# Kernel optimization log

Hardware: AMD Instinct MI355X
Metric: run time of the kernel (lower is better)

## Reference

```python
import jax, jax.numpy as jnp
import numpy as np

EPS = 1e-12  # torch F.normalize eps

def _l2norm(t):
    # normalize over last axis (tokens N), matching F.normalize(dim=-1)
    n = jnp.sqrt(jnp.sum(t * t, axis=-1, keepdims=True))
    return t / jnp.maximum(n, EPS)

def setup_inputs() -> dict:
    key = jax.random.key(0)
    ks = jax.random.split(key, 4)
    B, N, C, H = 16, 3136, 768, 16
    x = jax.random.normal(ks[0], (B, N, C), dtype=jnp.float32)
    w_qkv = jax.random.normal(ks[1], (3 * C, C), dtype=jnp.float32) * (C ** -0.5)
    temperature = jnp.ones((H, 1, 1), dtype=jnp.float32)
    w_proj = jax.random.normal(ks[2], (C, C), dtype=jnp.float32) * (C ** -0.5)
    b_proj = jnp.zeros((C,), dtype=jnp.float32)
    return {"x": x, "w_qkv": w_qkv, "temperature": temperature,
            "w_proj": w_proj, "b_proj": b_proj}

def reference(x, w_qkv, temperature, w_proj, b_proj):
    B, N, C = x.shape
    H = temperature.shape[0]
    dh = C // H
    # qkv: [B,N,3C] -> [B,N,3,H,dh] -> [3,B,H,dh,N]
    qkv = (x @ w_qkv.T).reshape(B, N, 3, H, dh)
    qkv = jnp.transpose(qkv, (2, 0, 3, 4, 1))
    q, k, v = qkv[0], qkv[1], qkv[2]          # each [B,H,dh,N]
    q = _l2norm(q)
    k = _l2norm(k)
    # cross-covariance attention over channel axis: [B,H,dh,dh]
    attn = jnp.einsum('bhdn,bhen->bhde', q, k) * temperature
    attn = jax.nn.softmax(attn, axis=-1)
    out = jnp.einsum('bhde,bhen->bhdn', attn, v)  # [B,H,dh,N]
    out = jnp.transpose(out, (0, 3, 1, 2)).reshape(B, N, C)
    return out @ w_proj.T + b_proj
```

## Files before the change

### kernel.cpp

```cpp
#include <hip/hip_runtime.h>
#include <hip/hip_bf16.h>
#include <stdint.h>

using f32x4   = __attribute__((ext_vector_type(4))) float;
using half8   = __attribute__((ext_vector_type(8))) _Float16;
using float4v = __attribute__((ext_vector_type(4))) float;

typedef const __attribute__((address_space(1))) void gas_void;
typedef __attribute__((address_space(3))) void las_void;

__device__ __forceinline__ void gload_lds16(const void* gptr, void* lptr) {
  __builtin_amdgcn_global_load_lds((gas_void*)(uintptr_t)gptr,
                                   (las_void*)(uintptr_t)lptr, 16, 0, 0);
}

#define MFMA_F16(a, b, c) __builtin_amdgcn_mfma_f32_16x16x32_f16((a), (b), (c), 0, 0, 0)

__global__ void k_cvt4(const float* __restrict__ x, const float* __restrict__ wqkv,
                       const float* __restrict__ wproj,
                       _Float16* __restrict__ x16, _Float16* __restrict__ w16,
                       _Float16* __restrict__ wp16, _Float16* __restrict__ wvT) {
  const long N0 = 4816896L, N1 = 221184L, N2 = 73728L, N3 = 98304L;
  const long total = N0 + N1 + N2 + N3;
  for (long i = (long)blockIdx.x * blockDim.x + threadIdx.x; i < total;
       i += (long)gridDim.x * blockDim.x) {
    if (i < N0 + N1 + N2) {
      const float* src; _Float16* dst; long off;
      if (i < N0)            { src = x;     dst = x16;  off = i; }
      else if (i < N0 + N1)  { src = wqkv;  dst = w16;  off = i - N0; }
      else                   { src = wproj; dst = wp16; off = i - N0 - N1; }
      const float4v* p = (const float4v*)(src + off * 8);
      float4v a = p[0], b = p[1];
      half8 o;
      o[0] = (_Float16)a[0]; o[1] = (_Float16)a[1]; o[2] = (_Float16)a[2]; o[3] = (_Float16)a[3];
      o[4] = (_Float16)b[0]; o[5] = (_Float16)b[1]; o[6] = (_Float16)b[2]; o[7] = (_Float16)b[3];
      *(half8*)(dst + off * 8) = o;
    } else {
      const long u = i - (N0 + N1 + N2);
      const int h = (int)(u / 6144);
      const int r = (int)(u % 6144);
      const int f = r >> 3, e0 = (r & 7) * 8;
      half8 o;
      if (e0 >= 48) {
#pragma unroll
        for (int j = 0; j < 8; ++j) o[j] = (_Float16)0.f;
      } else {
#pragma unroll
        for (int j = 0; j < 8; ++j)
          o[j] = (_Float16)wqkv[(long)(1536 + h * 48 + e0 + j) * 768 + f];
      }
      *(half8*)(wvT + ((long)(h * 768 + f) * 64 + e0)) = o;
    }
  }
}

template<bool OUT_F32>
__global__ __launch_bounds__(512, 2)
void k_gemm8p(const _Float16* __restrict__ A, const _Float16* __restrict__ B,
              void* __restrict__ Cv, const float* __restrict__ bias,
              int Mt, int Nt, long Areal, long Astr, long Bstr, long Cstr,
              long N, long K)
{
  __shared__ _Float16 lds[65536];
  const int tid  = threadIdx.x;
  const int wv   = tid >> 6, lane = tid & 63;
  const int g    = lane >> 4, cidx = lane & 15;
  const int wr   = wv >> 2, wc = wv & 3;

  const int nwg = (int)gridDim.x;
  const int q = nwg >> 3, r = nwg & 7;
  const int xcd = (int)blockIdx.x & 7, bidx = (int)blockIdx.x >> 3;
  int wg = (xcd < r ? xcd * (q + 1) : r * (q + 1) + (xcd - r) * q) + bidx;

  const int tpb = Mt * Nt;
  const int b   = wg / tpb;
  const int rem = wg - b * tpb;
  const long mt = rem % Mt, nt = rem / Mt;
  const long m0 = mt * 256, n0 = nt * 256;

  const int NT = (int)(K >> 6);
  const int NI = NT >> 1;

  const _Float16* Ab = A + b * Astr + m0 * K;
  const _Float16* Bb = B + b * Bstr + n0 * K;

  const int srow = lane >> 2;
  const int sgr  = (lane & 3) ^ ((lane >> 3) & 3);

  auto stage = [&](int op, int buf, int kh, int t) {
    const _Float16* src = op ? Bb : Ab;
    const long koff = (long)t * 64 + kh * 32 + sgr * 8;
#pragma unroll
    for (int l = 0; l < 2; ++l) {
      const int chunk = l * 8 + wv;
      gload_lds16(src + (long)(chunk * 16 + srow) * K + koff,
                  &lds[buf * 32768 + op * 16384 + kh * 8192 + chunk * 512]);
    }
  };

  const int gr  = (g ^ ((cidx >> 1) & 3)) * 8;
  const int raA = (wr * 128 + cidx) * 32 + gr;
  const int raB = 16384 + (wc * 64 + cidx) * 32 + gr;

  f32x4 acc[8][4] = {};

  stage(0, 0, 0, 0); stage(1, 0, 0, 0);
  stage(0, 0, 1, 0); stage(1, 0, 1, 0);
  stage(0, 1, 0, 1); stage(1, 1, 0, 1);
  asm volatile("s_waitcnt vmcnt(4)" ::: "memory");
  __builtin_amdgcn_sched_barrier(0);
  __builtin_amdgcn_s_barrier();

  half8 afA[4], afB[4], bfA[4], bfB[4];
#pragma unroll
  for (int mm = 0; mm < 4; ++mm) afA[mm] = *(const half8*)&lds[raA + mm * 512];
#pragma unroll
  for (int nn = 0; nn < 4; ++nn) bfA[nn] = *(const half8*)&lds[raB + nn * 512];

#define XPH(CURA, CURB, MLO, NA, NBUF, NKS, NMLO, LOADB, NB, STAGE, BDRY)      \
  {                                                                            \
    STAGE;                                                                     \
    if (BDRY) {                                                                \
      asm volatile("s_waitcnt vmcnt(4)" ::: "memory");                         \
      __builtin_amdgcn_sched_barrier(0);                                       \
    }                                                                          \
    __builtin_amdgcn_s_barrier();                                              \
    _Pragma("unroll")                                                          \
    for (int mm = 0; mm < 4; ++mm)                                             \
      NA[mm] = *(const half8*)&lds[(NBUF)*32768 + (NKS)*8192 + raA + ((NMLO)+mm)*512]; \
    if (LOADB) {                                                               \
      _Pragma("unroll")                                                        \
      for (int nn = 0; nn < 4; ++nn)                                           \
        NB[nn] = *(const half8*)&lds[(NBUF)*32768 + (NKS)*8192 + raB + nn*512]; \
    }                                                                          \
    __builtin_amdgcn_sched_barrier(0);                                         \
    __builtin_amdgcn_s_setprio(1);                                             \
    _Pragma("unroll")                                                          \
    for (int mm = 0; mm < 4; ++mm)                                             \
      _Pragma("unroll")                                                        \
      for (int nn = 0; nn < 4; ++nn)                                           \
        acc[(MLO)+mm][nn] = MFMA_F16(CURA[mm], CURB[nn], acc[(MLO)+mm][nn]);   \
    __builtin_amdgcn_s_setprio(0);                                             \
    __builtin_amdgcn_s_barrier();                                              \
  }

  for (int it = 0; it < NI; ++it) {
    const int t1c = 2 * it + 1;
    int tn2 = 2 * it + 2; if (tn2 >= NT) tn2 -= NT;
    int tn3 = 2 * it + 3; if (tn3 >= NT) tn3 -= NT;
    XPH(afA, bfA, 0, afB, 0, 0, 4, 0, bfB, stage(0, 1, 1, t1c), false)
    XPH(afB, bfA, 4, afA, 0, 1, 0, 1, bfB, stage(1, 1, 1, t1c), false)
    XPH(afA, bfB, 0, afB, 0, 1, 4, 0, bfA, stage(0, 0, 0, tn2), false)
    XPH(afB, bfB, 4, afA, 1, 0, 0, 1, bfA, stage(1, 0, 0, tn2), true )
    XPH(afA, bfA, 0, afB, 1, 0, 4, 0, bfB, stage(0, 0, 1, tn2), false)
    XPH(afB, bfA, 4, afA, 1, 1, 0, 1, bfB, stage(1, 0, 1, tn2), false)
    XPH(afA, bfB, 0, afB, 1, 1, 4, 0, bfA, stage(0, 1, 0, tn3), false)
    XPH(afB, bfB, 4, afA, 0, 0, 0, 1, bfA, stage(1, 1, 0, tn3), true )
  }
#undef XPH

  float bv[4] = {0.f, 0.f, 0.f, 0.f};
  if (bias) {
#pragma unroll
    for (int n = 0; n < 4; ++n) bv[n] = bias[n0 + wc * 64 + n * 16 + cidx];
  }
  if constexpr (OUT_F32) {
    float* C = (float*)Cv + b * Cstr;
#pragma unroll
    for (int m = 0; m < 8; ++m)
#pragma unroll
      for (int rr = 0; rr < 4; ++rr) {
        const long row = m0 + wr * 128 + m * 16 + g * 4 + rr;
        if (row < Areal) {
#pragma unroll
          for (int n = 0; n < 4; ++n)
            C[row * N + (n0 + wc * 64 + n * 16 + cidx)] = acc[m][n][rr] + bv[n];
        }
      }
  } else {
    _Float16* C = (_Float16*)Cv + b * Cstr;
#pragma unroll
    for (int m = 0; m < 8; ++m)
#pragma unroll
      for (int rr = 0; rr < 4; ++rr) {
        const long row = m0 + wr * 128 + m * 16 + g * 4 + rr;
        if (row < Areal) {
#pragma unroll
          for (int n = 0; n < 4; ++n)
            C[row * N + (n0 + wc * 64 + n * 16 + cidx)] = (_Float16)acc[m][n][rr];
        }
      }
  }
}

__global__ __launch_bounds__(256)
void k_wfin(const _Float16* __restrict__ Ag, const _Float16* __restrict__ Bg,
            _Float16* __restrict__ Cg)
{
  __shared__ _Float16 lds[2][2][128 * 32];
  const int tid  = threadIdx.x;
  const int wv   = tid >> 6, lane = tid & 63;
  const int g    = lane >> 4, cidx = lane & 15;
  const int wr   = wv >> 1, wc = wv & 1;

  const int nwg = (int)gridDim.x;
  const int q = nwg >> 3, r = nwg & 7;
  const int xcd = (int)blockIdx.x & 7, bidx = (int)blockIdx.x >> 3;
  const int wg  = (xcd < r ? xcd * (q + 1) : r * (q + 1) + (xcd - r) * q) + bidx;

  const int b = wg / 36, rem = wg % 36;
  const int mt = rem % 6, nt = rem / 6;
  const _Float16* Ab = Ag + (long)mt * 128 * 768;
  const _Float16* Bb = Bg + (long)b * 589824 + (long)nt * 128 * 768;
  _Float16* C = Cg + (long)b * 589824;

  const int srow = lane >> 2;
  const int sgr  = (lane & 3) ^ ((lane >> 3) & 3);

  auto stage = [&](int buf, int kt) {
#pragma unroll
    for (int i = 0; i < 2; ++i) {
      const int chunk = wv * 2 + i;
      const long go = (long)(chunk * 16 + srow) * 768 + (long)kt * 32 + sgr * 8;
      gload_lds16(Ab + go, &lds[buf][0][chunk * 512]);
      gload_lds16(Bb + go, &lds[buf][1][chunk * 512]);
    }
  };

  const int gr = (g ^ ((cidx >> 1) & 3)) * 8;

  f32x4 acc[4][4] = {};
  stage(0, 0);
  __syncthreads();
  for (int kt = 0; kt < 24; ++kt) {
    const int cur = kt & 1;
    if (kt + 1 < 24) stage(cur ^ 1, kt + 1);
    const _Float16* la = &lds[cur][0][0];
    const _Float16* lb = &lds[cur][1][0];
    half8 af[4], bf[4];
#pragma unroll
    for (int m = 0; m < 4; ++m)
      af[m] = *(const half8*)&la[(wr * 64 + m * 16 + cidx) * 32 + gr];
#pragma unroll
    for (int n = 0; n < 4; ++n)
      bf[n] = *(const half8*)&lb[(wc * 64 + n * 16 + cidx) * 32 + gr];
#pragma unroll
    for (int m = 0; m < 4; ++m)
#pragma unroll
      for (int n = 0; n < 4; ++n)
        acc[m][n] = MFMA_F16(af[m], bf[n], acc[m][n]);
    __syncthreads();
  }
#pragma unroll
  for (int m = 0; m < 4; ++m)
#pragma unroll
    for (int rr = 0; rr < 4; ++rr) {
      const long row = mt * 128 + wr * 64 + m * 16 + g * 4 + rr;
#pragma unroll
      for (int n = 0; n < 4; ++n)
        C[row * 768 + (nt * 128 + wc * 64 + n * 16 + cidx)] = (_Float16)acc[m][n][rr];
    }
}

__global__ __launch_bounds__(256)
void k_heads(const _Float16* __restrict__ qk,
             const _Float16* __restrict__ wvT,
             const float* __restrict__ temperature,
             _Float16* __restrict__ weffT)
{
  const int b = blockIdx.x >> 4;
  const int h = blockIdx.x & 15;
  const int tid = threadIdx.x;
  const int w = tid >> 6, lane = tid & 63;
  const int g = lane >> 4, c = lane & 15;
  const long T = 50176;
  const long tb = (long)b * 3136;

  __shared__ float red[4][48 * 48];
  __shared__ float redss[4][2][48];
  __shared__ float inv[2][48];
  __shared__ _Float16 Pb[48 * 64];

  f32x4 sqk[3][3] = {};
  f32x4 sqq[3] = {};
  f32x4 skk[3] = {};

  const _Float16* qbase = qk + (long)(h * 48) * T + tb;
  const _Float16* kbase = qk + (long)(768 + h * 48) * T + tb;

  for (int chunk = w; chunk < 49; chunk += 4) {
    const int t0 = chunk * 64;
    half8 qf[3][2], kf[3][2];
#pragma unroll
    for (int m = 0; m < 3; ++m)
#pragma unroll
      for (int ks = 0; ks < 2; ++ks) {
        const long off = (long)(m * 16 + c) * T + t0 + ks * 32 + g * 8;
        qf[m][ks] = *(const half8*)(qbase + off);
        kf[m][ks] = *(const half8*)(kbase + off);
      }
#pragma unroll
    for (int ks = 0; ks < 2; ++ks)
#pragma unroll
      for (int m = 0; m < 3; ++m) {
        sqq[m] = MFMA_F16(qf[m][ks], qf[m][ks], sqq[m]);
        skk[m] = MFMA_F16(kf[m][ks], kf[m][ks], skk[m]);
#pragma unroll
        for (int n = 0; n < 3; ++n)
          sqk[m][n] = MFMA_F16(qf[m][ks], kf[n][ks], sqk[m][n]);
      }
  }

#pragma unroll
  for (int m = 0; m < 3; ++m) {
#pragma unroll
    for (int n = 0; n < 3; ++n)
#pragma unroll
      for (int r = 0; r < 4; ++r)
        red[w][(m * 16 + g * 4 + r) * 48 + n * 16 + c] = sqk[m][n][r];
#pragma unroll
    for (int r = 0; r < 4; ++r)
      if (c == g * 4 + r) {
        redss[w][0][m * 16 + c] = sqq[m][r];
        redss[w][1][m * 16 + c] = skk[m][r];
      }
  }
  __syncthreads();

  if (tid < 96) {
    const int is_k = tid / 48, d = tid % 48;
    const float s = redss[0][is_k][d] + redss[1][is_k][d] + redss[2][is_k][d] + redss[3][is_k][d];
    inv[is_k][d] = 1.0f / fmaxf(sqrtf(s), 1e-12f);
  }
  __syncthreads();

  if (tid < 48) {
    const int d = tid;
    const float iq = inv[0][d] * temperature[h];
    float rowv[48];
    float mx = -3.0e38f;
#pragma unroll
    for (int e = 0; e < 48; ++e) {
      const int idx = d * 48 + e;
      float t = (red[0][idx] + red[1][idx] + red[2][idx] + red[3][idx]) * iq * inv[1][e];
      rowv[e] = t;
      mx = fmaxf(mx, t);
    }
    float sum = 0.f;
#pragma unroll
    for (int e = 0; e < 48; ++e) {
      const float p = __expf(rowv[e] - mx);
      rowv[e] = p;
      sum += p;
    }
    const float is = 1.0f / sum;
#pragma unroll
    for (int e = 0; e < 48; ++e)
      Pb[d * 64 + e] = (_Float16)(rowv[e] * is);
#pragma unroll
    for (int e = 48; e < 64; ++e)
      Pb[d * 64 + e] = (_Float16)0.f;
  }
  __syncthreads();

  half8 pf[3][2];
#pragma unroll
  for (int nf = 0; nf < 3; ++nf)
#pragma unroll
    for (int ks = 0; ks < 2; ++ks)
      pf[nf][ks] = *(const half8*)&Pb[(nf * 16 + c) * 64 + ks * 32 + g * 8];

  const _Float16* wvh = wvT + (long)h * 768 * 64;
  _Float16* wout = weffT + (long)b * 589824 + h * 48;

  for (int m = 0; m < 12; ++m) {
    const int f0 = w * 192 + m * 16;
    half8 va[2];
#pragma unroll
    for (int ks = 0; ks < 2; ++ks)
      va[ks] = *(const half8*)&wvh[(long)(f0 + c) * 64 + ks * 32 + g * 8];
    f32x4 a3[3] = {};
#pragma unroll
    for (int ks = 0; ks < 2; ++ks)
#pragma unroll
      for (int nf = 0; nf < 3; ++nf)
        a3[nf] = MFMA_F16(va[ks], pf[nf][ks], a3[nf]);
#pragma unroll
    for (int nf = 0; nf < 3; ++nf)
#pragma unroll
      for (int r = 0; r < 4; ++r)
        wout[(long)(f0 + g * 4 + r) * 768 + nf * 16 + c] = (_Float16)a3[nf][r];
  }
}

extern "C" void kernel_launch(void* const* d_in, const int* in_sizes, int n_in,
                              void* d_out, int out_size, void* d_ws, size_t ws_size,
                              hipStream_t stream)
{
  (void)in_sizes; (void)n_in; (void)out_size; (void)ws_size;
  const float* x      = (const float*)d_in[0];
  const float* w_qkv  = (const float*)d_in[1];
  const float* temp   = (const float*)d_in[2];
  const float* w_proj = (const float*)d_in[3];
  const float* b_proj = (const float*)d_in[4];
  float* out = (float*)d_out;

  char* ws = (char*)d_ws;
  _Float16* x16   = (_Float16*)(ws);
  _Float16* qkbuf = (_Float16*)(ws + 77070336L);
  _Float16* weffT = (_Float16*)(ws + 231211008L);
  _Float16* wfin  = (_Float16*)(ws + 250085376L);
  _Float16* w16   = (_Float16*)(ws + 268959744L);
  _Float16* wp16  = (_Float16*)(ws + 272498688L);
  _Float16* wvT   = (_Float16*)(ws + 273678336L);

  k_cvt4<<<2048, 256, 0, stream>>>(x, w_qkv, w_proj, x16, w16, wp16, wvT);
  k_gemm8p<false><<<1176, 512, 0, stream>>>(w16, x16, qkbuf, nullptr,
                                            6, 196, 1536, 0, 0, 0, 50176, 768);
  k_heads<<<256, 256, 0, stream>>>(qkbuf, wvT, temp, weffT);
  k_wfin<<<576, 256, 0, stream>>>(wp16, weffT, wfin);
  k_gemm8p<true><<<624, 512, 0, stream>>>(x16, wfin, out, b_proj,
                                          13, 3, 3136, 3136L * 768, 589824, 3136L * 768,
                                          768, 768);
}
```

Measured before the change: 365.9 us.

## Compute q·k and norms via per-batch Gram matrix of x instead of materializing QK

Replaces the large QK projection GEMM (1536x50176x768) with a per-batch symmetric Gram matrix G = xᵀx (768x768, computed over tokens), then forms Wq·G and Wk·G to get qᵀk and the q/k squared norms algebraically. Adds a transpose-and-convert kernel for x and swaps the 256-tile pipelined GEMM for a simpler 128-tile double-buffered GEMM used for all remaining GEMMs. This cuts the FLOPs and the large qk intermediate traffic, but it loses the hand-tuned pipelined GEMM for the final projection and adds an fp16 Gram accumulation whose precision may be a risk.

```diff
diff --git a/kernel.cpp b/kernel.cpp
--- a/kernel.cpp
+++ b/kernel.cpp
@@ -4,6 +4,7 @@
 
 using f32x4   = __attribute__((ext_vector_type(4))) float;
 using half8   = __attribute__((ext_vector_type(8))) _Float16;
+using half4   = __attribute__((ext_vector_type(4))) _Float16;
 using float4v = __attribute__((ext_vector_type(4))) float;
 
 typedef const __attribute__((address_space(1))) void gas_void;
@@ -16,19 +17,17 @@
 
 #define MFMA_F16(a, b, c) __builtin_amdgcn_mfma_f32_16x16x32_f16((a), (b), (c), 0, 0, 0)
 
-__global__ void k_cvt4(const float* __restrict__ x, const float* __restrict__ wqkv,
-                       const float* __restrict__ wproj,
-                       _Float16* __restrict__ x16, _Float16* __restrict__ w16,
-                       _Float16* __restrict__ wp16, _Float16* __restrict__ wvT) {
-  const long N0 = 4816896L, N1 = 221184L, N2 = 73728L, N3 = 98304L;
-  const long total = N0 + N1 + N2 + N3;
+__global__ void k_cvtw(const float* __restrict__ wqkv, const float* __restrict__ wproj,
+                       _Float16* __restrict__ w16, _Float16* __restrict__ wp16,
+                       _Float16* __restrict__ wvT) {
+  const long N1 = 221184L, N2 = 73728L, N3 = 98304L;
+  const long total = N1 + N2 + N3;
   for (long i = (long)blockIdx.x * blockDim.x + threadIdx.x; i < total;
        i += (long)gridDim.x * blockDim.x) {
-    if (i < N0 + N1 + N2) {
+    if (i < N1 + N2) {
       const float* src; _Float16* dst; long off;
-      if (i < N0)            { src = x;     dst = x16;  off = i; }
-      else if (i < N0 + N1)  { src = wqkv;  dst = w16;  off = i - N0; }
-      else                   { src = wproj; dst = wp16; off = i - N0 - N1; }
+      if (i < N1) { src = wqkv;  dst = w16;  off = i; }
+      else        { src = wproj; dst = wp16; off = i - N1; }
       const float4v* p = (const float4v*)(src + off * 8);
       float4v a = p[0], b = p[1];
       half8 o;
@@ -36,7 +35,7 @@
       o[4] = (_Float16)b[0]; o[5] = (_Float16)b[1]; o[6] = (_Float16)b[2]; o[7] = (_Float16)b[3];
       *(half8*)(dst + off * 8) = o;
     } else {
-      const long u = i - (N0 + N1 + N2);
+      const long u = i - N1 - N2;
       const int h = (int)(u / 6144);
       const int r = (int)(u % 6144);
       const int f = r >> 3, e0 = (r & 7) * 8;
@@ -54,110 +53,182 @@
   }
 }
 
-template<bool OUT_F32>
-__global__ __launch_bounds__(512, 2)
-void k_gemm8p(const _Float16* __restrict__ A, const _Float16* __restrict__ B,
-              void* __restrict__ Cv, const float* __restrict__ bias,
-              int Mt, int Nt, long Areal, long Astr, long Bstr, long Cstr,
-              long N, long K)
-{
-  __shared__ _Float16 lds[65536];
-  const int tid  = threadIdx.x;
-  const int wv   = tid >> 6, lane = tid & 63;
-  const int g    = lane >> 4, cidx = lane & 15;
-  const int wr   = wv >> 2, wc = wv & 3;
+__global__ __launch_bounds__(256)
+void k_cvtx(const float* __restrict__ x, _Float16* __restrict__ x16,
+            _Float16* __restrict__ xT) {
+  __shared__ _Float16 lt[64 * 68];
+  const int bid = blockIdx.x;
+  const int b = bid / 588;
+  const int rem = bid % 588;
+  const int tt = rem / 12, ct = rem % 12;
+  const long t0g = (long)b * 3136 + tt * 64;
+  const int c0 = ct * 64;
+  const int tid = threadIdx.x;
+#pragma unroll
+  for (int ch = 0; ch < 4; ++ch) {
+    const int idx = tid + ch * 256;
+    const int tr = idx >> 4, cg = (idx & 15) * 4;
+    float4v v = *(const float4v*)&x[(t0g + tr) * 768 + c0 + cg];
+    half4 hv;
+    hv[0] = (_Float16)v[0]; hv[1] = (_Float16)v[1];
+    hv[2] = (_Float16)v[2]; hv[3] = (_Float16)v[3];
+    *(half4*)&x16[(t0g + tr) * 768 + c0 + cg] = hv;
+    *(half4*)&lt[tr * 68 + cg] = hv;
+  }
+  __syncthreads();
+  const int c = tid >> 2, tch = tid & 3;
+  half8 o0, o1;
+#pragma unroll
+  for (int j = 0; j < 8; ++j) o0[j] = lt[(tch * 16 + j) * 68 + c];
+#pragma unroll
+  for (int j = 0; j < 8; ++j) o1[j] = lt[(tch * 16 + 8 + j) * 68 + c];
+  _Float16* dst = xT + (long)b * 2408448 + (long)(c0 + c) * 3136 + tt * 64 + tch * 16;
+  *(half8*)dst = o0;
+  *(half8*)(dst + 8) = o1;
+}
+
+__global__ __launch_bounds__(256)
+void k_gram(const _Float16* __restrict__ xT, _Float16* __restrict__ G) {
+  __shared__ _Float16 lds[2][2][128 * 32];
+  const int tid = threadIdx.x;
+  const int wv = tid >> 6, lane = tid & 63;
+  const int g = lane >> 4, cidx = lane & 15;
+  const int wr = wv >> 1, wc = wv & 1;
 
   const int nwg = (int)gridDim.x;
   const int q = nwg >> 3, r = nwg & 7;
   const int xcd = (int)blockIdx.x & 7, bidx = (int)blockIdx.x >> 3;
   int wg = (xcd < r ? xcd * (q + 1) : r * (q + 1) + (xcd - r) * q) + bidx;
-
+  const int b = wg / 21;
+  int p = wg % 21;
+  int mt = 0;
+  while (p >= 6 - mt) { p -= 6 - mt; ++mt; }
+  const int nt = mt + p;
+
+  const _Float16* Ab = xT + (long)b * 2408448 + (long)mt * 128 * 3136;
+  const _Float16* Bb = xT + (long)b * 2408448 + (long)nt * 128 * 3136;
+
+  const int srow = lane >> 2;
+  const int sgr  = (lane & 3) ^ ((lane >> 3) & 3);
+
+  auto stage = [&](int buf, int kt) {
+#pragma unroll
+    for (int l = 0; l < 2; ++l) {
+      const int rbase = wv * 32 + l * 16;
+      const long koff = (long)kt * 32 + sgr * 8;
+      gload_lds16(Ab + (long)(rbase + srow) * 3136 + koff, &lds[buf][0][rbase * 32]);
+      gload_lds16(Bb + (long)(rbase + srow) * 3136 + koff, &lds[buf][1][rbase * 32]);
+    }
+  };
+  const int gr = (g ^ ((cidx >> 1) & 3)) * 8;
+
+  f32x4 acc[4][4] = {};
+  stage(0, 0);
+  __syncthreads();
+  for (int kt = 0; kt < 98; ++kt) {
+    const int cur = kt & 1;
+    if (kt + 1 < 98) stage(cur ^ 1, kt + 1);
+    half8 af[4], bf[4];
+#pragma unroll
+    for (int m = 0; m < 4; ++m)
+      af[m] = *(const half8*)&lds[cur][0][(wr * 64 + m * 16 + cidx) * 32 + gr];
+#pragma unroll
+    for (int n = 0; n < 4; ++n)
+      bf[n] = *(const half8*)&lds[cur][1][(wc * 64 + n * 16 + cidx) * 32 + gr];
+#pragma unroll
+    for (int m = 0; m < 4; ++m)
+#pragma unroll
+      for (int n = 0; n < 4; ++n)
+        acc[m][n] = MFMA_F16(af[m], bf[n], acc[m][n]);
+    __syncthreads();
+  }
+  _Float16* Gb = G + (long)b * 589824;
+  const long m0 = (long)mt * 128, n0 = (long)nt * 128;
+#pragma unroll
+  for (int m = 0; m < 4; ++m)
+#pragma unroll
+    for (int rr = 0; rr < 4; ++rr) {
+      const long row = m0 + wr * 64 + m * 16 + g * 4 + rr;
+#pragma unroll
+      for (int n = 0; n < 4; ++n)
+        Gb[row * 768 + n0 + wc * 64 + n * 16 + cidx] = (_Float16)acc[m][n][rr];
+    }
+  if (mt != nt) {
+#pragma unroll
+    for (int m = 0; m < 4; ++m)
+#pragma unroll
+      for (int n = 0; n < 4; ++n) {
+        half4 hv;
+#pragma unroll
+        for (int rr = 0; rr < 4; ++rr) hv[rr] = (_Float16)acc[m][n][rr];
+        const long col  = n0 + wc * 64 + n * 16 + cidx;
+        const long row0 = m0 + wr * 64 + m * 16 + g * 4;
+        *(half4*)&Gb[col * 768 + row0] = hv;
+      }
+  }
+}
+
+template<bool OUT_F32>
+__global__ __launch_bounds__(256)
+void k_g128(const _Float16* __restrict__ A, const _Float16* __restrict__ B,
+            void* __restrict__ Cv, const float* __restrict__ bias,
+            int Mt, int Nt, long Areal, long Astr, long Bstr, long Cstr,
+            long N, long K)
+{
+  __shared__ _Float16 lds[2][2][128 * 32];
+  const int tid = threadIdx.x;
+  const int wv = tid >> 6, lane = tid & 63;
+  const int g = lane >> 4, cidx = lane & 15;
+  const int wr = wv >> 1, wc = wv & 1;
+
+  const int nwg = (int)gridDim.x;
+  const int q = nwg >> 3, r = nwg & 7;
+  const int xcd = (int)blockIdx.x & 7, bidx = (int)blockIdx.x >> 3;
+  int wg = (xcd < r ? xcd * (q + 1) : r * (q + 1) + (xcd - r) * q) + bidx;
   const int tpb = Mt * Nt;
-  const int b   = wg / tpb;
-  const int rem = wg - b * tpb;
-  const long mt = rem % Mt, nt = rem / Mt;
-  const long m0 = mt * 256, n0 = nt * 256;
-
-  const int NT = (int)(K >> 6);
-  const int NI = NT >> 1;
+  const int b = wg / tpb;
+  const int rem = wg % tpb;
+  const int mt = rem % Mt, nt = rem / Mt;
+  const long m0 = (long)mt * 128, n0 = (long)nt * 128;
 
   const _Float16* Ab = A + b * Astr + m0 * K;
   const _Float16* Bb = B + b * Bstr + n0 * K;
+  const int nkt = (int)(K >> 5);
 
   const int srow = lane >> 2;
   const int sgr  = (lane & 3) ^ ((lane >> 3) & 3);
 
-  auto stage = [&](int op, int buf, int kh, int t) {
-    const _Float16* src = op ? Bb : Ab;
-    const long koff = (long)t * 64 + kh * 32 + sgr * 8;
+  auto stage = [&](int buf, int kt) {
 #pragma unroll
     for (int l = 0; l < 2; ++l) {
-      const int chunk = l * 8 + wv;
-      gload_lds16(src + (long)(chunk * 16 + srow) * K + koff,
-                  &lds[buf * 32768 + op * 16384 + kh * 8192 + chunk * 512]);
+      const int rbase = wv * 32 + l * 16;
+      const long koff = (long)kt * 32 + sgr * 8;
+      gload_lds16(Ab + (long)(rbase + srow) * K + koff, &lds[buf][0][rbase * 32]);
+      gload_lds16(Bb + (long)(rbase + srow) * K + koff, &lds[buf][1][rbase * 32]);
     }
   };
-
-  const int gr  = (g ^ ((cidx >> 1) & 3)) * 8;
-  const int raA = (wr * 128 + cidx) * 32 + gr;
-  const int raB = 16384 + (wc * 64 + cidx) * 32 + gr;
-
-  f32x4 acc[8][4] = {};
-
-  stage(0, 0, 0, 0); stage(1, 0, 0, 0);
-  stage(0, 0, 1, 0); stage(1, 0, 1, 0);
-  stage(0, 1, 0, 1); stage(1, 1, 0, 1);
-  asm volatile("s_waitcnt vmcnt(4)" ::: "memory");
-  __builtin_amdgcn_sched_barrier(0);
-  __builtin_amdgcn_s_barrier();
-
-  half8 afA[4], afB[4], bfA[4], bfB[4];
-#pragma unroll
-  for (int mm = 0; mm < 4; ++mm) afA[mm] = *(const half8*)&lds[raA + mm * 512];
-#pragma unroll
-  for (int nn = 0; nn < 4; ++nn) bfA[nn] = *(const half8*)&lds[raB + nn * 512];
-
-#define XPH(CURA, CURB, MLO, NA, NBUF, NKS, NMLO, LOADB, NB, STAGE, BDRY)      \
-  {                                                                            \
-    STAGE;                                                                     \
-    if (BDRY) {                                                                \
-      asm volatile("s_waitcnt vmcnt(4)" ::: "memory");                         \
-      __builtin_amdgcn_sched_barrier(0);                                       \
-    }                                                                          \
-    __builtin_amdgcn_s_barrier();                                              \
-    _Pragma("unroll")                                                          \
-    for (int mm = 0; mm < 4; ++mm)                                             \
-      NA[mm] = *(const half8*)&lds[(NBUF)*32768 + (NKS)*8192 + raA + ((NMLO)+mm)*512]; \
-    if (LOADB) {                                                               \
-      _Pragma("unroll")                                                        \
-      for (int nn = 0; nn < 4; ++nn)                                           \
-        NB[nn] = *(const half8*)&lds[(NBUF)*32768 + (NKS)*8192 + raB + nn*512]; \
-    }                                                                          \
-    __builtin_amdgcn_sched_barrier(0);                                         \
-    __builtin_amdgcn_s_setprio(1);                                             \
-    _Pragma("unroll")                                                          \
-    for (int mm = 0; mm < 4; ++mm)                                             \
-      _Pragma("unroll")                                                        \
-      for (int nn = 0; nn < 4; ++nn)                                           \
-        acc[(MLO)+mm][nn] = MFMA_F16(CURA[mm], CURB[nn], acc[(MLO)+mm][nn]);   \
-    __builtin_amdgcn_s_setprio(0);                                             \
-    __builtin_amdgcn_s_barrier();                                              \
-  }
-
-  for (int it = 0; it < NI; ++it) {
-    const int t1c = 2 * it + 1;
-    int tn2 = 2 * it + 2; if (tn2 >= NT) tn2 -= NT;
-    int tn3 = 2 * it + 3; if (tn3 >= NT) tn3 -= NT;
-    XPH(afA, bfA, 0, afB, 0, 0, 4, 0, bfB, stage(0, 1, 1, t1c), false)
-    XPH(afB, bfA, 4, afA, 0, 1, 0, 1, bfB, stage(1, 1, 1, t1c), false)
-    XPH(afA, bfB, 0, afB, 0, 1, 4, 0, bfA, stage(0, 0, 0, tn2), false)
-    XPH(afB, bfB, 4, afA, 1, 0, 0, 1, bfA, stage(1, 0, 0, tn2), true )
-    XPH(afA, bfA, 0, afB, 1, 0, 4, 0, bfB, stage(0, 0, 1, tn2), false)
-    XPH(afB, bfA, 4, afA, 1, 1, 0, 1, bfB, stage(1, 0, 1, tn2), false)
-    XPH(afA, bfB, 0, afB, 1, 1, 4, 0, bfA, stage(0, 1, 0, tn3), false)
-    XPH(afB, bfB, 4, afA, 0, 0, 0, 1, bfA, stage(1, 1, 0, tn3), true )
-  }
-#undef XPH
+  const int gr = (g ^ ((cidx >> 1) & 3)) * 8;
+
+  f32x4 acc[4][4] = {};
+  stage(0, 0);
+  __syncthreads();
+  for (int kt = 0; kt < nkt; ++kt) {
+    const int cur = kt & 1;
+    if (kt + 1 < nkt) stage(cur ^ 1, kt + 1);
+    half8 af[4], bf[4];
+#pragma unroll
+    for (int m = 0; m < 4; ++m)
+      af[m] = *(const half8*)&lds[cur][0][(wr * 64 + m * 16 + cidx) * 32 + gr];
+#pragma unroll
+    for (int n = 0; n < 4; ++n)
+      bf[n] = *(const half8*)&lds[cur][1][(wc * 64 + n * 16 + cidx) * 32 + gr];
+#pragma unroll
+    for (int m = 0; m < 4; ++m)
+#pragma unroll
+      for (int n = 0; n < 4; ++n)
+        acc[m][n] = MFMA_F16(af[m], bf[n], acc[m][n]);
+    __syncthreads();
+  }
 
   float bv[4] = {0.f, 0.f, 0.f, 0.f};
   if (bias) {
@@ -167,148 +238,74 @@
   if constexpr (OUT_F32) {
     float* C = (float*)Cv + b * Cstr;
 #pragma unroll
-    for (int m = 0; m < 8; ++m)
+    for (int m = 0; m < 4; ++m)
 #pragma unroll
       for (int rr = 0; rr < 4; ++rr) {
-        const long row = m0 + wr * 128 + m * 16 + g * 4 + rr;
+        const long row = m0 + wr * 64 + m * 16 + g * 4 + rr;
         if (row < Areal) {
 #pragma unroll
           for (int n = 0; n < 4; ++n)
-            C[row * N + (n0 + wc * 64 + n * 16 + cidx)] = acc[m][n][rr] + bv[n];
+            C[row * N + n0 + wc * 64 + n * 16 + cidx] = acc[m][n][rr] + bv[n];
         }
       }
   } else {
     _Float16* C = (_Float16*)Cv + b * Cstr;
 #pragma unroll
-    for (int m = 0; m < 8; ++m)
+    for (int m = 0; m < 4; ++m)
 #pragma unroll
       for (int rr = 0; rr < 4; ++rr) {
-        const long row = m0 + wr * 128 + m * 16 + g * 4 + rr;
+        const long row = m0 + wr * 64 + m * 16 + g * 4 + rr;
         if (row < Areal) {
 #pragma unroll
           for (int n = 0; n < 4; ++n)
-            C[row * N + (n0 + wc * 64 + n * 16 + cidx)] = (_Float16)acc[m][n][rr];
+            C[row * N + n0 + wc * 64 + n * 16 + cidx] = (_Float16)acc[m][n][rr];
         }
       }
   }
 }
 
 __global__ __launch_bounds__(256)
-void k_wfin(const _Float16* __restrict__ Ag, const _Float16* __restrict__ Bg,
-            _Float16* __restrict__ Cg)
-{
-  __shared__ _Float16 lds[2][2][128 * 32];
-  const int tid  = threadIdx.x;
-  const int wv   = tid >> 6, lane = tid & 63;
-  const int g    = lane >> 4, cidx = lane & 15;
-  const int wr   = wv >> 1, wc = wv & 1;
-
-  const int nwg = (int)gridDim.x;
-  const int q = nwg >> 3, r = nwg & 7;
-  const int xcd = (int)blockIdx.x & 7, bidx = (int)blockIdx.x >> 3;
-  const int wg  = (xcd < r ? xcd * (q + 1) : r * (q + 1) + (xcd - r) * q) + bidx;
-
-  const int b = wg / 36, rem = wg % 36;
-  const int mt = rem % 6, nt = rem / 6;
-  const _Float16* Ab = Ag + (long)mt * 128 * 768;
-  const _Float16* Bb = Bg + (long)b * 589824 + (long)nt * 128 * 768;
-  _Float16* C = Cg + (long)b * 589824;
-
-  const int srow = lane >> 2;
-  const int sgr  = (lane & 3) ^ ((lane >> 3) & 3);
-
-  auto stage = [&](int buf, int kt) {
-#pragma unroll
-    for (int i = 0; i < 2; ++i) {
-      const int chunk = wv * 2 + i;
-      const long go = (long)(chunk * 16 + srow) * 768 + (long)kt * 32 + sgr * 8;
-      gload_lds16(Ab + go, &lds[buf][0][chunk * 512]);
-      gload_lds16(Bb + go, &lds[buf][1][chunk * 512]);
-    }
-  };
-
-  const int gr = (g ^ ((cidx >> 1) & 3)) * 8;
-
-  f32x4 acc[4][4] = {};
-  stage(0, 0);
-  __syncthreads();
-  for (int kt = 0; kt < 24; ++kt) {
-    const int cur = kt & 1;
-    if (kt + 1 < 24) stage(cur ^ 1, kt + 1);
-    const _Float16* la = &lds[cur][0][0];
-    const _Float16* lb = &lds[cur][1][0];
-    half8 af[4], bf[4];
-#pragma unroll
-    for (int m = 0; m < 4; ++m)
-      af[m] = *(const half8*)&la[(wr * 64 + m * 16 + cidx) * 32 + gr];
-#pragma unroll
-    for (int n = 0; n < 4; ++n)
-      bf[n] = *(const half8*)&lb[(wc * 64 + n * 16 + cidx) * 32 + gr];
-#pragma unroll
-    for (int m = 0; m < 4; ++m)
-#pragma unroll
-      for (int n = 0; n < 4; ++n)
-        acc[m][n] = MFMA_F16(af[m], bf[n], acc[m][n]);
-    __syncthreads();
-  }
-#pragma unroll
-  for (int m = 0; m < 4; ++m)
-#pragma unroll
-    for (int rr = 0; rr < 4; ++rr) {
-      const long row = mt * 128 + wr * 64 + m * 16 + g * 4 + rr;
-#pragma unroll
-      for (int n = 0; n < 4; ++n)
-        C[row * 768 + (nt * 128 + wc * 64 + n * 16 + cidx)] = (_Float16)acc[m][n][rr];
-    }
-}
-
-__global__ __launch_bounds__(256)
-void k_heads(const _Float16* __restrict__ qk,
-             const _Float16* __restrict__ wvT,
-             const float* __restrict__ temperature,
+void k_heads(const _Float16* __restrict__ QG, const _Float16* __restrict__ w16,
+             const _Float16* __restrict__ wvT, const float* __restrict__ temperature,
              _Float16* __restrict__ weffT)
 {
-  const int b = blockIdx.x >> 4;
-  const int h = blockIdx.x & 15;
+  const int b = blockIdx.x >> 4, h = blockIdx.x & 15;
   const int tid = threadIdx.x;
   const int w = tid >> 6, lane = tid & 63;
   const int g = lane >> 4, c = lane & 15;
-  const long T = 50176;
-  const long tb = (long)b * 3136;
 
   __shared__ float red[4][48 * 48];
   __shared__ float redss[4][2][48];
   __shared__ float inv[2][48];
   __shared__ _Float16 Pb[48 * 64];
 
-  f32x4 sqk[3][3] = {};
-  f32x4 sqq[3] = {};
-  f32x4 skk[3] = {};
-
-  const _Float16* qbase = qk + (long)(h * 48) * T + tb;
-  const _Float16* kbase = qk + (long)(768 + h * 48) * T + tb;
-
-  for (int chunk = w; chunk < 49; chunk += 4) {
-    const int t0 = chunk * 64;
-    half8 qf[3][2], kf[3][2];
-#pragma unroll
-    for (int m = 0; m < 3; ++m)
-#pragma unroll
-      for (int ks = 0; ks < 2; ++ks) {
-        const long off = (long)(m * 16 + c) * T + t0 + ks * 32 + g * 8;
-        qf[m][ks] = *(const half8*)(qbase + off);
-        kf[m][ks] = *(const half8*)(kbase + off);
-      }
-#pragma unroll
-    for (int ks = 0; ks < 2; ++ks)
-#pragma unroll
-      for (int m = 0; m < 3; ++m) {
-        sqq[m] = MFMA_F16(qf[m][ks], qf[m][ks], sqq[m]);
-        skk[m] = MFMA_F16(kf[m][ks], kf[m][ks], skk[m]);
-#pragma unroll
-        for (int n = 0; n < 3; ++n)
-          sqk[m][n] = MFMA_F16(qf[m][ks], kf[n][ks], sqk[m][n]);
-      }
+  const _Float16* QGq = QG + (long)b * 1179648 + (long)(h * 48) * 768;
+  const _Float16* QGk = QGq + 768L * 768;
+  const _Float16* Wq  = w16 + (long)(h * 48) * 768;
+  const _Float16* Wk  = w16 + (long)(768 + h * 48) * 768;
+
+  f32x4 aS[3][3] = {};
+  f32x4 aq[3] = {};
+  f32x4 ak[3] = {};
+  for (int ks = w * 6; ks < w * 6 + 6; ++ks) {
+    const int k0 = ks * 32 + g * 8;
+    half8 t1[3], t3[3], wqf[3], wkf[3];
+#pragma unroll
+    for (int m = 0; m < 3; ++m) {
+      const long ro = (long)(m * 16 + c) * 768 + k0;
+      t1[m]  = *(const half8*)(QGq + ro);
+      t3[m]  = *(const half8*)(QGk + ro);
+      wqf[m] = *(const half8*)(Wq + ro);
+      wkf[m] = *(const half8*)(Wk + ro);
+    }
+#pragma unroll
+    for (int m = 0; m < 3; ++m) {
+      aq[m] = MFMA_F16(t1[m], wqf[m], aq[m]);
+      ak[m] = MFMA_F16(t3[m], wkf[m], ak[m]);
+#pragma unroll
+      for (int n = 0; n < 3; ++n)
+        aS[m][n] = MFMA_F16(t1[m], wkf[n], aS[m][n]);
+    }
   }
 
 #pragma unroll
@@ -316,13 +313,13 @@
 #pragma unroll
     for (int n = 0; n < 3; ++n)
 #pragma unroll
-      for (int r = 0; r < 4; ++r)
-        red[w][(m * 16 + g * 4 + r) * 48 + n * 16 + c] = sqk[m][n][r];
-#pragma unroll
-    for (int r = 0; r < 4; ++r)
-      if (c == g * 4 + r) {
-        redss[w][0][m * 16 + c] = sqq[m][r];
-        redss[w][1][m * 16 + c] = skk[m][r];
+      for (int rr = 0; rr < 4; ++rr)
+        red[w][(m * 16 + g * 4 + rr) * 48 + n * 16 + c] = aS[m][n][rr];
+#pragma unroll
+    for (int rr = 0; rr < 4; ++rr)
+      if (c == g * 4 + rr) {
+        redss[w][0][m * 16 + c] = aq[m][rr];
+        redss[w][1][m * 16 + c] = ak[m][rr];
       }
   }
   __syncthreads();
@@ -349,9 +346,9 @@
     float sum = 0.f;
 #pragma unroll
     for (int e = 0; e < 48; ++e) {
-      const float p = __expf(rowv[e] - mx);
-      rowv[e] = p;
-      sum += p;
+      const float pv = __expf(rowv[e] - mx);
+      rowv[e] = pv;
+      sum += pv;
     }
     const float is = 1.0f / sum;
 #pragma unroll
@@ -388,8 +385,8 @@
 #pragma unroll
     for (int nf = 0; nf < 3; ++nf)
 #pragma unroll
-      for (int r = 0; r < 4; ++r)
-        wout[(long)(f0 + g * 4 + r) * 768 + nf * 16 + c] = (_Float16)a3[nf][r];
+      for (int rr = 0; rr < 4; ++rr)
+        wout[(long)(f0 + g * 4 + rr) * 768 + nf * 16 + c] = (_Float16)a3[nf][rr];
   }
 }
 
@@ -407,19 +404,24 @@
 
   char* ws = (char*)d_ws;
   _Float16* x16   = (_Float16*)(ws);
-  _Float16* qkbuf = (_Float16*)(ws + 77070336L);
-  _Float16* weffT = (_Float16*)(ws + 231211008L);
-  _Float16* wfin  = (_Float16*)(ws + 250085376L);
-  _Float16* w16   = (_Float16*)(ws + 268959744L);
-  _Float16* wp16  = (_Float16*)(ws + 272498688L);
-  _Float16* wvT   = (_Float16*)(ws + 273678336L);
-
-  k_cvt4<<<2048, 256, 0, stream>>>(x, w_qkv, w_proj, x16, w16, wp16, wvT);
-  k_gemm8p<false><<<1176, 512, 0, stream>>>(w16, x16, qkbuf, nullptr,
-                                            6, 196, 1536, 0, 0, 0, 50176, 768);
-  k_heads<<<256, 256, 0, stream>>>(qkbuf, wvT, temp, weffT);
-  k_wfin<<<576, 256, 0, stream>>>(wp16, weffT, wfin);
-  k_gemm8p<true><<<624, 512, 0, stream>>>(x16, wfin, out, b_proj,
-                                          13, 3, 3136, 3136L * 768, 589824, 3136L * 768,
-                                          768, 768);
-}
+  _Float16* xT    = (_Float16*)(ws + 77070336L);
+  _Float16* G     = (_Float16*)(ws + 154140672L);
+  _Float16* QG    = (_Float16*)(ws + 173015040L);
+  _Float16* weffT = (_Float16*)(ws + 210763776L);
+  _Float16* wfin  = (_Float16*)(ws + 229638144L);
+  _Float16* w16   = (_Float16*)(ws + 248512512L);
+  _Float16* wp16  = (_Float16*)(ws + 252051456L);
+  _Float16* wvT   = (_Float16*)(ws + 253231104L);
+
+  k_cvtw<<<768, 256, 0, stream>>>(w_qkv, w_proj, w16, wp16, wvT);
+  k_cvtx<<<9408, 256, 0, stream>>>(x, x16, xT);
+  k_gram<<<336, 256, 0, stream>>>(xT, G);
+  k_g128<false><<<1152, 256, 0, stream>>>(w16, G, QG, nullptr,
+                                          12, 6, 1536, 0, 589824, 1179648, 768, 768);
+  k_heads<<<256, 256, 0, stream>>>(QG, w16, wvT, temp, weffT);
+  k_g128<false><<<576, 256, 0, stream>>>(wp16, weffT, wfin, nullptr,
+                                         6, 6, 768, 0, 589824, 589824, 768, 768);
+  k_g128<true><<<2400, 256, 0, stream>>>(x16, wfin, out, b_proj,
+                                         25, 6, 3136, 3136L * 768, 589824, 3136L * 768,
+                                         768, 768);
+}
```

Measured after the change: 339.9 us. 1.08x faster.
